# Optimization experiments

Hardware: AMD Instinct MI355X
Metric: run time of the kernel (lower is better)

## Reference

```python
import jax, jax.numpy as jnp
import numpy as np

NA, NW, H = 20000, 100000, 128
DA, DW = 64, 128
E_CR, E_IN, E_CO = 400000, 600000, 300000


def _seg_softmax(logits, seg, n):
    m = jax.ops.segment_max(logits, seg, num_segments=n)
    e = jnp.exp(logits - m[seg])
    s = jax.ops.segment_sum(e, seg, num_segments=n)
    return e / (s[seg] + 1e-16)


def _gat(x_src, x_dst, edge, W, b, a_s, a_d):
    # PyG GATConv, heads=1, concat=False, shared lin for src/dst, add_self_loops=True
    n_src, n_dst = x_src.shape[0], x_dst.shape[0]
    loops = jnp.arange(min(n_src, n_dst), dtype=edge.dtype)
    src = jnp.concatenate([edge[0], loops])
    dst = jnp.concatenate([edge[1], loops])
    hs = x_src @ W            # [n_src, H]
    hd = x_dst @ W            # [n_dst, H]
    logit = jax.nn.leaky_relu((hs @ a_s)[src] + (hd @ a_d)[dst], 0.2)
    alpha = _seg_softmax(logit, dst, n_dst)          # softmax over in-neighborhoods
    out = jax.ops.segment_sum(alpha[:, None] * hs[src], dst, num_segments=n_dst)
    return out + b


def _mlp2(x, w1, b1, w2, b2):
    return jax.nn.relu(x @ w1 + b1) @ w2 + b2


def setup_inputs() -> dict:
    key = jax.random.key(0)
    ks = iter(jax.random.split(key, 40))

    def p(shape, scale=0.1):
        return jax.random.normal(next(ks), shape, jnp.float32) * scale

    def edges(n_src, n_dst, E):
        s = jax.random.randint(next(ks), (E,), 0, n_src, dtype=jnp.int32)
        d = jax.random.randint(next(ks), (E,), 0, n_dst, dtype=jnp.int32)
        d = jnp.where(s == d, (d + 1) % n_dst, d)  # keep input loop-free (PyG strips them)
        return jnp.stack([s, d])

    e_creates = edges(NA, NW, E_CR)
    inp = {
        'artist_feat': jax.random.normal(next(ks), (NA, DA), jnp.float32),
        'work_feat': jax.random.normal(next(ks), (NW, DW), jnp.float32),
        'a_w1': p((DA, H)), 'a_b1': jnp.zeros(H, jnp.float32),
        'a_w2': p((H, H)), 'a_b2': jnp.zeros(H, jnp.float32),
        'w_w1': p((DW, H)), 'w_b1': jnp.zeros(H, jnp.float32),
        'w_w2': p((H, H)), 'w_b2': jnp.zeros(H, jnp.float32),
        'cr_W': p((H, H)), 'cr_b': jnp.zeros(H, jnp.float32), 'cr_as': p((H,)), 'cr_ad': p((H,)),
        'in_W': p((H, H)), 'in_b': jnp.zeros(H, jnp.float32), 'in_as': p((H,)), 'in_ad': p((H,)),
        'co_W': p((H, H)), 'co_b': jnp.zeros(H, jnp.float32), 'co_as': p((H,)), 'co_ad': p((H,)),
        'p_w1': p((2 * H, 256)), 'p_b1': jnp.zeros(256, jnp.float32),
        'p_w2': p((256, 128)), 'p_b2': jnp.zeros(128, jnp.float32),
        'p_w3': p((128, 1)), 'p_b3': jnp.zeros(1, jnp.float32),
        'e_creates': e_creates,
        'e_created_by': jnp.flip(e_creates, axis=0),  # reverse relation [work, artist]
        'e_infl': edges(NW, NW, E_IN),
        'e_collab': edges(NA, NA, E_CO),
    }
    return inp


def reference(artist_feat, work_feat,
              a_w1, a_b1, a_w2, a_b2,
              w_w1, w_b1, w_w2, w_b2,
              cr_W, cr_b, cr_as, cr_ad,
              in_W, in_b, in_as, in_ad,
              co_W, co_b, co_as, co_ad,
              p_w1, p_b1, p_w2, p_b2, p_w3, p_b3,
              e_creates, e_created_by, e_infl, e_collab):
    ax = _mlp2(artist_feat, a_w1, a_b1, a_w2, a_b2)      # [NA, H]
    wx = _mlp2(work_feat, w_w1, w_b1, w_w2, w_b2)        # [NW, H]
    wx = jax.nn.elu(_gat(ax, wx, e_creates, cr_W, cr_b, cr_as, cr_ad))
    wx = jax.nn.elu(_gat(wx, wx, e_infl, in_W, in_b, in_as, in_ad))
    au = _gat(wx, ax, e_created_by, cr_W, cr_b, cr_as, cr_ad)  # no elu (matches source)
    ac = jax.nn.elu(_gat(au, au, e_collab, co_W, co_b, co_as, co_ad))
    comb = jnp.concatenate([au, ac], axis=1)             # [NA, 2H]
    h = jax.nn.relu(comb @ p_w1 + p_b1)                  # dropout is identity in eval
    h = jax.nn.relu(h @ p_w2 + p_b2)
    return (h @ p_w3 + p_b3).squeeze()
```

## Files before the change

kernel.cpp:

```cpp
#include <hip/hip_runtime.h>
#include <hip/hip_bf16.h>
#include <cstddef>

#define NA 20000
#define NW 100000
#define HH 128
#define DA 64
#define E_CR 400000
#define E_IN 600000
#define E_CO 300000

#define ROW1 0
#define ROW2 (NW)
#define ROW3 (2 * NW)
#define ROW4 (2 * NW + NA)
#define NTOT (2 * NW + 2 * NA)
#define ETOTR (E_CR + E_IN + E_CR + E_CO)
#define CAPW 40
#define CAPA 88
#define NPREP (10 * 128 + 1)

typedef short v8s __attribute__((ext_vector_type(8)));
typedef float v4f __attribute__((ext_vector_type(4)));

constexpr int PSLOT = 2 * 128 * 264;

__device__ inline short f2bf(float x) {
    union { float f; unsigned u; } c; c.f = x;
    unsigned r = c.u + 0x7fff + ((c.u >> 16) & 1);
    return (short)(r >> 16);
}
__device__ inline float bf2f(short s) {
    union { unsigned u; float f; } c; c.u = ((unsigned)(unsigned short)s) << 16;
    return c.f;
}
__device__ inline float bfu2f(unsigned short s) {
    union { unsigned u; float f; } c; c.u = ((unsigned)s) << 16;
    return c.f;
}

__device__ inline void split8(const float* xv, v8s& h, v8s& l) {
#pragma unroll
    for (int p = 0; p < 4; ++p) {
        float2 xf; xf.x = xv[2 * p]; xf.y = xv[2 * p + 1];
        __hip_bfloat162 hb = __float22bfloat162_rn(xf);
        float2 hf = __bfloat1622float2(hb);
        float2 lf; lf.x = xf.x - hf.x; lf.y = xf.y - hf.y;
        __hip_bfloat162 lb = __float22bfloat162_rn(lf);
        union { __hip_bfloat162 b; short2 s; } uh, ul;
        uh.b = hb; ul.b = lb;
        h[2 * p] = uh.s.x; h[2 * p + 1] = uh.s.y;
        l[2 * p] = ul.s.x; l[2 * p + 1] = ul.s.y;
    }
}

struct PrepDesc { const float* src; int ldw; int K; };
struct PrepArgs { PrepDesc d[10]; const float* wvW; const float* wvA; float* vd; };
struct EdgeSets { const int* e[4]; int E[4]; int row[4]; int cum[5]; int* pad[4]; int cap[4]; };

__global__ __launch_bounds__(256) void k_prep_append(PrepArgs a, short* __restrict__ out,
                                                    EdgeSets es, int* __restrict__ deg)
{
    if (blockIdx.x < NPREP) {
        if (blockIdx.x == NPREP - 1) {
            __shared__ float sa[HH];
            int t = threadIdx.x;
            if (t < HH) sa[t] = a.wvA[t];
            __syncthreads();
            if (t < HH) {
                float s = 0.f;
                for (int jj = 0; jj < HH; ++jj) s += a.wvW[(size_t)t * HH + jj] * sa[jj];
                a.vd[t] = s;
            }
            return;
        }
        int m = blockIdx.x >> 7;
        int e = (blockIdx.x & 127) * 256 + threadIdx.x;
        PrepDesc dd = a.d[m];
        int K = dd.K;
        int KP = (K <= 128) ? K + 8 : K;
        if (e >= K * 128) return;
        int n = e & 127, k = e >> 7;
        float x = dd.src[(size_t)k * dd.ldw + n];
        short h = f2bf(x);
        short l = f2bf(x - bf2f(h));
        short* base = out + (size_t)m * PSLOT;
        base[n * KP + k] = h;
        base[128 * KP + n * KP + k] = l;
        return;
    }
    int b0 = (blockIdx.x - NPREP) * 1024 + threadIdx.x;
    int s[4], d[4], g[4]; bool ok[4];
#pragma unroll
    for (int u = 0; u < 4; ++u) {
        int i = b0 + u * 256;
        ok[u] = i < es.cum[4];
        s[u] = 0; d[u] = 0; g[u] = 0;
        if (ok[u]) {
            int gi = (i >= es.cum[1]) + (i >= es.cum[2]) + (i >= es.cum[3]);
            int t = i - es.cum[gi];
            s[u] = es.e[gi][t];
            d[u] = es.e[gi][es.E[gi] + t];
            g[u] = gi;
        }
    }
    int p[4];
#pragma unroll
    for (int u = 0; u < 4; ++u) if (ok[u]) p[u] = atomicAdd(&deg[es.row[g[u]] + d[u]], 1);
#pragma unroll
    for (int u = 0; u < 4; ++u)
        if (ok[u] && p[u] < es.cap[g[u]])
            es.pad[g[u]][(size_t)d[u] * es.cap[g[u]] + p[u]] = s[u];
}

template<int K, int ACT, int NSS, int ST, int LDSB, int OBF, int DUAL>
__global__ __launch_bounds__(256, 2) void k_mfma(
    const float* __restrict__ X, int ldx,
    const short* __restrict__ Wp,
    const float* __restrict__ bias,
    float* __restrict__ Y, int ldy, int M,
    const float* __restrict__ v1, float* __restrict__ ss1,
    const float* __restrict__ v2, float* __restrict__ ss2,
    const float* __restrict__ sb)
{
    constexpr int KF = K / 32;
    constexpr int KP = LDSB ? K + 8 : K;
    __shared__ short Bs[LDSB ? 2 * 128 * (K + 8) : 8];
    const int tid = threadIdx.x;
    const int wave = tid >> 6, lane = tid & 63;
    const int l15 = lane & 15, quad = lane >> 4;
    int bid = blockIdx.x;
    if (DUAL) {
        int g0 = gridDim.x >> 1;
        if (bid >= g0) { bid -= g0; Wp += PSLOT; bias += 128; Y += 128; }
    }
    const int wrow = bid * 128 + wave * 32;

    if (LDSB) {
        const float4* src = (const float4*)Wp;
        float4* dst = (float4*)Bs;
        constexpr int total = 2 * 128 * KP / 8;
        for (int i = tid; i < total; i += 256) dst[i] = src[i];
    }

    v4f acc[2][8];
#pragma unroll
    for (int rf = 0; rf < 2; ++rf)
#pragma unroll
        for (int cf = 0; cf < 8; ++cf) acc[rf][cf] = (v4f){0.f, 0.f, 0.f, 0.f};

    if (LDSB) {
        v8s ah[2][KF], al[2][KF];
#pragma unroll
        for (int rf = 0; rf < 2; ++rf) {
            int r = wrow + rf * 16 + l15; if (r >= M) r = M - 1;
            const float* xp = X + (size_t)r * ldx + quad * 8;
#pragma unroll
            for (int kf = 0; kf < KF; ++kf) {
                float xv[8];
                *(float4*)&xv[0] = *(const float4*)(xp + kf * 32);
                *(float4*)&xv[4] = *(const float4*)(xp + kf * 32 + 4);
                split8(xv, ah[rf][kf], al[rf][kf]);
            }
        }
        __syncthreads();
#pragma unroll
        for (int kf = 0; kf < KF; ++kf) {
#pragma unroll
            for (int cf = 0; cf < 8; ++cf) {
                const short* bp = &Bs[(cf * 16 + l15) * KP + kf * 32 + quad * 8];
                v8s bh = *(const v8s*)bp;
                v8s bl = *(const v8s*)(bp + 128 * KP);
#pragma unroll
                for (int rf = 0; rf < 2; ++rf) {
                    acc[rf][cf] = __builtin_amdgcn_mfma_f32_16x16x32_bf16(al[rf][kf], bh, acc[rf][cf], 0, 0, 0);
                    acc[rf][cf] = __builtin_amdgcn_mfma_f32_16x16x32_bf16(ah[rf][kf], bl, acc[rf][cf], 0, 0, 0);
                    acc[rf][cf] = __builtin_amdgcn_mfma_f32_16x16x32_bf16(ah[rf][kf], bh, acc[rf][cf], 0, 0, 0);
                }
            }
        }
    } else {
        for (int kf = 0; kf < KF; ++kf) {
            v8s ah[2], al[2];
#pragma unroll
            for (int rf = 0; rf < 2; ++rf) {
                int r = wrow + rf * 16 + l15; if (r >= M) r = M - 1;
                const float* xp = X + (size_t)r * ldx + kf * 32 + quad * 8;
                float xv[8];
                *(float4*)&xv[0] = *(const float4*)xp;
                *(float4*)&xv[4] = *(const float4*)(xp + 4);
                split8(xv, ah[rf], al[rf]);
            }
#pragma unroll
            for (int cf = 0; cf < 8; ++cf) {
                const short* bp = Wp + (size_t)(cf * 16 + l15) * K + kf * 32 + quad * 8;
                v8s bh = *(const v8s*)bp;
                v8s bl = *(const v8s*)(bp + 128 * KP);
#pragma unroll
                for (int rf = 0; rf < 2; ++rf) {
                    acc[rf][cf] = __builtin_amdgcn_mfma_f32_16x16x32_bf16(al[rf], bh, acc[rf][cf], 0, 0, 0);
                    acc[rf][cf] = __builtin_amdgcn_mfma_f32_16x16x32_bf16(ah[rf], bl, acc[rf][cf], 0, 0, 0);
                    acc[rf][cf] = __builtin_amdgcn_mfma_f32_16x16x32_bf16(ah[rf], bh, acc[rf][cf], 0, 0, 0);
                }
            }
        }
    }

    float bv[8], v1c[8], v2c[8];
#pragma unroll
    for (int cf = 0; cf < 8; ++cf) {
        int col = cf * 16 + l15;
        bv[cf] = bias ? bias[col] : 0.f;
        if (NSS >= 1) v1c[cf] = v1[col];
        if (NSS >= 2) v2c[cf] = v2[col];
    }
    float sbv = (NSS >= 1 && sb) ? sb[0] : 0.f;

#pragma unroll
    for (int rf = 0; rf < 2; ++rf) {
#pragma unroll
        for (int reg = 0; reg < 4; ++reg) {
            int r = wrow + rf * 16 + quad * 4 + reg;
            if (r >= M) continue;
            float p1 = 0.f, p2 = 0.f;
#pragma unroll
            for (int cf = 0; cf < 8; ++cf) {
                float o = acc[rf][cf][reg] + bv[cf];
                if (ACT == 1) o = o > 0.f ? o : 0.f;
                if (NSS >= 1) p1 = fmaf(o, v1c[cf], p1);
                if (NSS >= 2) p2 = fmaf(o, v2c[cf], p2);
                if (ST) {
                    if (OBF) ((unsigned short*)Y)[(size_t)r * ldy + cf * 16 + l15] = (unsigned short)f2bf(o);
                    else     Y[(size_t)r * ldy + cf * 16 + l15] = o;
                }
            }
            if (NSS >= 1) {
#pragma unroll
                for (int w = 1; w < 16; w <<= 1) {
                    p1 += __shfl_xor(p1, w, 64);
                    if (NSS >= 2) p2 += __shfl_xor(p2, w, 64);
                }
                if (l15 == 0) {
                    ss1[r] = p1 + sbv;
                    if (NSS >= 2) ss2[r] = p2;
                }
            }
        }
    }
}

struct MfmaCfg {
    const float* X; int ldx;
    const short* Wp;
    const float* bias;
    float* Y; int ldy; int M;
    int act, nss, obf;
    const float* v1; float* ss1;
    const float* v2; float* ss2;
    int nblocks;
};

__global__ __launch_bounds__(256, 2) void k_mfma2(MfmaCfg c0, MfmaCfg c1)
{
    constexpr int K = 128, KF = 4, KP = 136;
    __shared__ short Bs[2 * 128 * KP];
    const bool first = blockIdx.x < c0.nblocks;
    const MfmaCfg& c = first ? c0 : c1;
    const int bid = first ? blockIdx.x : blockIdx.x - c0.nblocks;
    const int tid = threadIdx.x;
    const int wave = tid >> 6, lane = tid & 63;
    const int l15 = lane & 15, quad = lane >> 4;
    const int wrow = bid * 128 + wave * 32;

    {
        const float4* src = (const float4*)c.Wp;
        float4* dst = (float4*)Bs;
        constexpr int total = 2 * 128 * KP / 8;
        for (int i = tid; i < total; i += 256) dst[i] = src[i];
    }

    v4f acc[2][8];
#pragma unroll
    for (int rf = 0; rf < 2; ++rf)
#pragma unroll
        for (int cf = 0; cf < 8; ++cf) acc[rf][cf] = (v4f){0.f, 0.f, 0.f, 0.f};

    v8s ah[2][KF], al[2][KF];
#pragma unroll
    for (int rf = 0; rf < 2; ++rf) {
        int r = wrow + rf * 16 + l15; if (r >= c.M) r = c.M - 1;
        const float* xp = c.X + (size_t)r * c.ldx + quad * 8;
#pragma unroll
        for (int kf = 0; kf < KF; ++kf) {
            float xv[8];
            *(float4*)&xv[0] = *(const float4*)(xp + kf * 32);
            *(float4*)&xv[4] = *(const float4*)(xp + kf * 32 + 4);
            split8(xv, ah[rf][kf], al[rf][kf]);
        }
    }
    __syncthreads();
#pragma unroll
    for (int kf = 0; kf < KF; ++kf) {
#pragma unroll
        for (int cf = 0; cf < 8; ++cf) {
            const short* bp = &Bs[(cf * 16 + l15) * KP + kf * 32 + quad * 8];
            v8s bh = *(const v8s*)bp;
            v8s bl = *(const v8s*)(bp + 128 * KP);
#pragma unroll
            for (int rf = 0; rf < 2; ++rf) {
                acc[rf][cf] = __builtin_amdgcn_mfma_f32_16x16x32_bf16(al[rf][kf], bh, acc[rf][cf], 0, 0, 0);
                acc[rf][cf] = __builtin_amdgcn_mfma_f32_16x16x32_bf16(ah[rf][kf], bl, acc[rf][cf], 0, 0, 0);
                acc[rf][cf] = __builtin_amdgcn_mfma_f32_16x16x32_bf16(ah[rf][kf], bh, acc[rf][cf], 0, 0, 0);
            }
        }
    }

    float bv[8], v1c[8], v2c[8];
#pragma unroll
    for (int cf = 0; cf < 8; ++cf) {
        int col = cf * 16 + l15;
        bv[cf] = c.bias ? c.bias[col] : 0.f;
        v1c[cf] = (c.nss >= 1) ? c.v1[col] : 0.f;
        v2c[cf] = (c.nss >= 2) ? c.v2[col] : 0.f;
    }

#pragma unroll
    for (int rf = 0; rf < 2; ++rf) {
#pragma unroll
        for (int reg = 0; reg < 4; ++reg) {
            int r = wrow + rf * 16 + quad * 4 + reg;
            if (r >= c.M) continue;
            float p1 = 0.f, p2 = 0.f;
#pragma unroll
            for (int cf = 0; cf < 8; ++cf) {
                float o = acc[rf][cf][reg] + bv[cf];
                if (c.act) o = o > 0.f ? o : 0.f;
                p1 = fmaf(o, v1c[cf], p1);
                p2 = fmaf(o, v2c[cf], p2);
                if (c.obf) ((unsigned short*)c.Y)[(size_t)r * c.ldy + cf * 16 + l15] = (unsigned short)f2bf(o);
                else       c.Y[(size_t)r * c.ldy + cf * 16 + l15] = o;
            }
            if (c.nss >= 1) {
#pragma unroll
                for (int w = 1; w < 16; w <<= 1) {
                    p1 += __shfl_xor(p1, w, 64);
                    p2 += __shfl_xor(p2, w, 64);
                }
                if (l15 == 0) {
                    c.ss1[r] = p1;
                    if (c.nss >= 2) c.ss2[r] = p2;
                }
            }
        }
    }
}

template<int ELU, int U, int CAP>
__global__ __launch_bounds__(256) void k_aggregate(
    const int* __restrict__ deg, const int* __restrict__ esp,
    const unsigned short* __restrict__ hs, const float* __restrict__ ss,
    const float* __restrict__ sd, const float* __restrict__ bias,
    float* __restrict__ out, int ldy, int n, int loopn)
{
    int lane = threadIdx.x & 63;
    int wv = threadIdx.x >> 6;
    int d = blockIdx.x * 4 + wv;
    if (d >= n) return;
    int half = lane >> 5;
    int col = (lane & 31) * 4;
    const int* row = esp + (size_t)d * CAP;
    int i1 = deg[d]; if (i1 > CAP) i1 = CAP;
    float sdv = sd[d];
    float den = 0.f;
    float ax = 0.f, ay = 0.f, az = 0.f, aw = 0.f;
    if (half == 0 && d < loopn) {
        ushort4 h = *(const ushort4*)(hs + (size_t)d * HH + col);
        float l = ss[d] + sdv;
        l = l < 0.f ? 0.2f * l : l;
        float e = __expf(l);
        den += e;
        ax = fmaf(e, bfu2f(h.x), ax);
        ay = fmaf(e, bfu2f(h.y), ay);
        az = fmaf(e, bfu2f(h.z), az);
        aw = fmaf(e, bfu2f(h.w), aw);
    }
    int i = 0;
    for (; i + 2 * U <= i1; i += 2 * U) {
        int s[U]; ushort4 h[U]; float sv[U];
#pragma unroll
        for (int u = 0; u < U; ++u) s[u] = row[i + 2 * u + half];
#pragma unroll
        for (int u = 0; u < U; ++u) h[u] = *(const ushort4*)(hs + (size_t)s[u] * HH + col);
#pragma unroll
        for (int u = 0; u < U; ++u) sv[u] = ss[s[u]];
#pragma unroll
        for (int u = 0; u < U; ++u) {
            float l = sv[u] + sdv;
            l = l < 0.f ? 0.2f * l : l;
            float e = __expf(l);
            den += e;
            ax = fmaf(e, bfu2f(h[u].x), ax);
            ay = fmaf(e, bfu2f(h[u].y), ay);
            az = fmaf(e, bfu2f(h[u].z), az);
            aw = fmaf(e, bfu2f(h[u].w), aw);
        }
    }
    if (i < i1) {
        int s[U]; ushort4 h[U]; float sv[U]; bool act[U];
#pragma unroll
        for (int u = 0; u < U; ++u) {
            int idx = i + 2 * u + half;
            act[u] = idx < i1;
            s[u] = row[act[u] ? idx : (i1 - 1)];
        }
#pragma unroll
        for (int u = 0; u < U; ++u) h[u] = *(const ushort4*)(hs + (size_t)s[u] * HH + col);
#pragma unroll
        for (int u = 0; u < U; ++u) sv[u] = ss[s[u]];
#pragma unroll
        for (int u = 0; u < U; ++u) {
            float l = sv[u] + sdv;
            l = l < 0.f ? 0.2f * l : l;
            float e = act[u] ? __expf(l) : 0.f;
            den += e;
            ax = fmaf(e, bfu2f(h[u].x), ax);
            ay = fmaf(e, bfu2f(h[u].y), ay);
            az = fmaf(e, bfu2f(h[u].z), az);
            aw = fmaf(e, bfu2f(h[u].w), aw);
        }
    }
    den += __shfl_xor(den, 32, 64);
    ax += __shfl_xor(ax, 32, 64);
    ay += __shfl_xor(ay, 32, 64);
    az += __shfl_xor(az, 32, 64);
    aw += __shfl_xor(aw, 32, 64);
    if (half == 0) {
        float4 b = *(const float4*)(bias + col);
        float inv = 1.f / (den + 1e-16f);
        float o0 = ax * inv + b.x;
        float o1 = ay * inv + b.y;
        float o2 = az * inv + b.z;
        float o3 = aw * inv + b.w;
        if (ELU) {
            o0 = o0 > 0.f ? o0 : expm1f(o0);
            o1 = o1 > 0.f ? o1 : expm1f(o1);
            o2 = o2 > 0.f ? o2 : expm1f(o2);
            o3 = o3 > 0.f ? o3 : expm1f(o3);
        }
        *(float4*)(out + (size_t)d * ldy + col) = make_float4(o0, o1, o2, o3);
    }
}

extern "C" void kernel_launch(void* const* d_in, const int* in_sizes, int n_in,
                              void* d_out, int out_size, void* d_ws, size_t ws_size,
                              hipStream_t stream)
{
    const float* artist = (const float*)d_in[0];
    const float* workf  = (const float*)d_in[1];
    const float* a_w1 = (const float*)d_in[2];  const float* a_b1 = (const float*)d_in[3];
    const float* a_w2 = (const float*)d_in[4];  const float* a_b2 = (const float*)d_in[5];
    const float* w_w1 = (const float*)d_in[6];  const float* w_b1 = (const float*)d_in[7];
    const float* w_w2 = (const float*)d_in[8];  const float* w_b2 = (const float*)d_in[9];
    const float* cr_W = (const float*)d_in[10]; const float* cr_b = (const float*)d_in[11];
    const float* cr_as = (const float*)d_in[12]; const float* cr_ad = (const float*)d_in[13];
    const float* in_W = (const float*)d_in[14]; const float* in_b = (const float*)d_in[15];
    const float* in_as = (const float*)d_in[16]; const float* in_ad = (const float*)d_in[17];
    const float* co_W = (const float*)d_in[18]; const float* co_b = (const float*)d_in[19];
    const float* co_as = (const float*)d_in[20]; const float* co_ad = (const float*)d_in[21];
    const float* p_w1 = (const float*)d_in[22]; const float* p_b1 = (const float*)d_in[23];
    const float* p_w2 = (const float*)d_in[24]; const float* p_b2 = (const float*)d_in[25];
    const float* p_w3 = (const float*)d_in[26]; const float* p_b3 = (const float*)d_in[27];
    const int* e_cr = (const int*)d_in[28];
    const int* e_cb = (const int*)d_in[29];
    const int* e_in = (const int*)d_in[30];
    const int* e_co = (const int*)d_in[31];

    char* wsp = (char*)d_ws;
    size_t off = 0;
    auto alloc = [&](size_t bytes) -> void* {
        void* p = wsp + off;
        off += (bytes + 255) / 256 * 256;
        return p;
    };
    float* ax   = (float*)alloc((size_t)NA * HH * 4);
    float* hsA  = (float*)alloc((size_t)NA * HH * 4);
    float* wx   = (float*)alloc((size_t)NW * HH * 4);
    float* hs   = (float*)alloc((size_t)NW * HH * 4);
    unsigned short* hsb = (unsigned short*)alloc((size_t)NW * HH * 2);
    float* comb = (float*)alloc((size_t)NA * 256 * 4);
    float* ss1 = (float*)alloc((size_t)NA * 4);
    float* sd1 = (float*)alloc((size_t)NW * 4);
    float* ss2 = (float*)alloc((size_t)NW * 4);
    float* sd2 = (float*)alloc((size_t)NW * 4);
    float* ss3 = (float*)alloc((size_t)NW * 4);
    float* sd3 = (float*)alloc((size_t)NA * 4);
    float* ss4 = (float*)alloc((size_t)NA * 4);
    float* sd4 = (float*)alloc((size_t)NA * 4);
    float* vd  = (float*)alloc(HH * 4);
    int* deg   = (int*)alloc((size_t)NTOT * 4);
    int* pad1  = (int*)alloc((size_t)NW * CAPW * 4);
    int* pad2  = (int*)alloc((size_t)NW * CAPW * 4);
    int* pad3  = (int*)alloc((size_t)NA * CAPA * 4);
    int* pad4  = (int*)alloc((size_t)NA * CAPA * 4);
    short* preW = (short*)alloc((size_t)10 * PSLOT * 2);
    (void)ws_size; (void)in_sizes; (void)n_in; (void)out_size;

    auto pre = [&](int m) { return preW + (size_t)m * PSLOT; };
    auto gg = [](int M) { return (M + 127) / 128; };
    const float* nf = nullptr;
    float* nfm = nullptr;

    PrepArgs pa;
    pa.d[0] = {a_w1, HH, DA};
    pa.d[1] = {a_w2, HH, HH};
    pa.d[2] = {w_w1, HH, HH};
    pa.d[3] = {w_w2, HH, HH};
    pa.d[4] = {cr_W, HH, HH};
    pa.d[5] = {in_W, HH, HH};
    pa.d[6] = {co_W, HH, HH};
    pa.d[7] = {p_w1, 256, 256};
    pa.d[8] = {p_w1 + 128, 256, 256};
    pa.d[9] = {p_w2, HH, 256};
    pa.wvW = cr_W; pa.wvA = cr_ad; pa.vd = vd;

    EdgeSets es;
    es.e[0] = e_cr; es.e[1] = e_in; es.e[2] = e_cb; es.e[3] = e_co;
    es.E[0] = E_CR; es.E[1] = E_IN; es.E[2] = E_CR; es.E[3] = E_CO;
    es.row[0] = ROW1; es.row[1] = ROW2; es.row[2] = ROW3; es.row[3] = ROW4;
    es.cum[0] = 0; es.cum[1] = E_CR; es.cum[2] = E_CR + E_IN;
    es.cum[3] = E_CR + E_IN + E_CR; es.cum[4] = ETOTR;
    es.pad[0] = pad1; es.pad[1] = pad2; es.pad[2] = pad3; es.pad[3] = pad4;
    es.cap[0] = CAPW; es.cap[1] = CAPW; es.cap[2] = CAPA; es.cap[3] = CAPA;

    (void)hipMemsetAsync(deg, 0, (size_t)NTOT * 4, stream);
    int nApp = (ETOTR + 1023) / 1024;
    k_prep_append<<<NPREP + nApp, 256, 0, stream>>>(pa, preW, es, deg);

    k_mfma<DA, 1, 0, 1, 1, 0, 0><<<gg(NA), 256, 0, stream>>>(artist, DA, pre(0), a_b1, hsA, HH, NA, nf, nfm, nf, nfm, nf);

    {
        MfmaCfg c0 = {workf, HH, pre(2), w_b1, hs, HH, NW, 1, 0, 0, nf, nfm, nf, nfm, gg(NW)};
        MfmaCfg c1 = {hsA, HH, pre(1), a_b2, ax, HH, NA, 0, 1, 0, vd, sd3, nf, nfm, gg(NA)};
        k_mfma2<<<gg(NW) + gg(NA), 256, 0, stream>>>(c0, c1);
    }
    {
        MfmaCfg c0 = {hs, HH, pre(3), w_b2, wx, HH, NW, 0, 1, 0, vd, sd1, nf, nfm, gg(NW)};
        MfmaCfg c1 = {ax, HH, pre(4), nullptr, (float*)hsb, HH, NA, 0, 1, 1, cr_as, ss1, nf, nfm, gg(NA)};
        k_mfma2<<<gg(NW) + gg(NA), 256, 0, stream>>>(c0, c1);
    }

    k_aggregate<1, 2, CAPW><<<(NW + 3) / 4, 256, 0, stream>>>(deg + ROW1, pad1, hsb, ss1, sd1, cr_b, wx, HH, NW, NA);

    k_mfma<HH, 0, 2, 1, 1, 1, 0><<<gg(NW), 256, 0, stream>>>(wx, HH, pre(5), nullptr, (float*)hsb, HH, NW, in_as, ss2, in_ad, sd2, nf);
    k_aggregate<1, 2, CAPW><<<(NW + 3) / 4, 256, 0, stream>>>(deg + ROW2, pad2, hsb, ss2, sd2, in_b, wx, HH, NW, NW);

    k_mfma<HH, 0, 1, 1, 1, 1, 0><<<gg(NW), 256, 0, stream>>>(wx, HH, pre(4), nullptr, (float*)hsb, HH, NW, cr_as, ss3, nf, nfm, nf);
    k_aggregate<0, 4, CAPA><<<(NA + 3) / 4, 256, 0, stream>>>(deg + ROW3, pad3, hsb, ss3, sd3, cr_b, comb, 256, NA, NA);

    k_mfma<HH, 0, 2, 1, 1, 1, 0><<<gg(NA), 256, 0, stream>>>(comb, 256, pre(6), nullptr, (float*)hsb, HH, NA, co_as, ss4, co_ad, sd4, nf);
    k_aggregate<1, 4, CAPA><<<(NA + 3) / 4, 256, 0, stream>>>(deg + ROW4, pad4, hsb, ss4, sd4, co_b, comb + 128, 256, NA, NA);

    float* h1 = hs;
    k_mfma<256, 1, 0, 1, 0, 0, 1><<<2 * gg(NA), 256, 0, stream>>>(comb, 256, pre(7), p_b1, h1, 256, NA, nf, nfm, nf, nfm, nf);
    k_mfma<256, 1, 1, 0, 0, 0, 0><<<gg(NA), 256, 0, stream>>>(h1, 256, pre(9), p_b2, nfm, 0, NA, p_w3, (float*)d_out, nf, nfm, p_b3);
}
```

Baseline: 617.7 us.

## Split edge-append across earlier kernels so each relation is built just in time

The single edge-bucketing pass over all four relations is split into per-relation chunks, and each chunk rides as extra blocks on a kernel that runs before that relation's aggregation (prep, the two dual-MFMA kernels, and the influence-GEMM now launched through the dual kernel). The goal is to shorten the serial prep step and let atomic scatter work overlap with MFMA GEMM blocks. It adds a branch and an extra kernel argument to the MFMA kernel, and mixing the two kinds of block may change occupancy.

```diff
diff --git a/kernel.cpp b/kernel.cpp
--- a/kernel.cpp
+++ b/kernel.cpp
@@ -15,7 +15,6 @@
 #define ROW3 (2 * NW)
 #define ROW4 (2 * NW + NA)
 #define NTOT (2 * NW + 2 * NA)
-#define ETOTR (E_CR + E_IN + E_CR + E_CO)
 #define CAPW 40
 #define CAPA 88
 #define NPREP (10 * 128 + 1)
@@ -54,63 +53,59 @@
     }
 }
 
+struct AppChunk { const int* e; int E; int* pad; int cap; int* deg; };
+
+__device__ inline void do_append(const AppChunk& ap, int bid) {
+    int b0 = bid * 1024 + threadIdx.x;
+    int s[4], d[4]; bool ok[4];
+#pragma unroll
+    for (int u = 0; u < 4; ++u) {
+        int i = b0 + u * 256;
+        ok[u] = i < ap.E;
+        s[u] = 0; d[u] = 0;
+        if (ok[u]) { s[u] = ap.e[i]; d[u] = ap.e[ap.E + i]; }
+    }
+    int p[4];
+#pragma unroll
+    for (int u = 0; u < 4; ++u) if (ok[u]) p[u] = atomicAdd(&ap.deg[d[u]], 1);
+#pragma unroll
+    for (int u = 0; u < 4; ++u)
+        if (ok[u] && p[u] < ap.cap)
+            ap.pad[(size_t)d[u] * ap.cap + p[u]] = s[u];
+}
+
 struct PrepDesc { const float* src; int ldw; int K; };
 struct PrepArgs { PrepDesc d[10]; const float* wvW; const float* wvA; float* vd; };
-struct EdgeSets { const int* e[4]; int E[4]; int row[4]; int cum[5]; int* pad[4]; int cap[4]; };
 
 __global__ __launch_bounds__(256) void k_prep_append(PrepArgs a, short* __restrict__ out,
-                                                    EdgeSets es, int* __restrict__ deg)
+                                                    AppChunk ap)
 {
-    if (blockIdx.x < NPREP) {
-        if (blockIdx.x == NPREP - 1) {
-            __shared__ float sa[HH];
-            int t = threadIdx.x;
-            if (t < HH) sa[t] = a.wvA[t];
-            __syncthreads();
-            if (t < HH) {
-                float s = 0.f;
-                for (int jj = 0; jj < HH; ++jj) s += a.wvW[(size_t)t * HH + jj] * sa[jj];
-                a.vd[t] = s;
-            }
-            return;
-        }
-        int m = blockIdx.x >> 7;
-        int e = (blockIdx.x & 127) * 256 + threadIdx.x;
-        PrepDesc dd = a.d[m];
-        int K = dd.K;
-        int KP = (K <= 128) ? K + 8 : K;
-        if (e >= K * 128) return;
-        int n = e & 127, k = e >> 7;
-        float x = dd.src[(size_t)k * dd.ldw + n];
-        short h = f2bf(x);
-        short l = f2bf(x - bf2f(h));
-        short* base = out + (size_t)m * PSLOT;
-        base[n * KP + k] = h;
-        base[128 * KP + n * KP + k] = l;
+    if (blockIdx.x >= NPREP) { do_append(ap, blockIdx.x - NPREP); return; }
+    if (blockIdx.x == NPREP - 1) {
+        __shared__ float sa[HH];
+        int t = threadIdx.x;
+        if (t < HH) sa[t] = a.wvA[t];
+        __syncthreads();
+        if (t < HH) {
+            float s = 0.f;
+            for (int jj = 0; jj < HH; ++jj) s += a.wvW[(size_t)t * HH + jj] * sa[jj];
+            a.vd[t] = s;
+        }
         return;
     }
-    int b0 = (blockIdx.x - NPREP) * 1024 + threadIdx.x;
-    int s[4], d[4], g[4]; bool ok[4];
-#pragma unroll
-    for (int u = 0; u < 4; ++u) {
-        int i = b0 + u * 256;
-        ok[u] = i < es.cum[4];
-        s[u] = 0; d[u] = 0; g[u] = 0;
-        if (ok[u]) {
-            int gi = (i >= es.cum[1]) + (i >= es.cum[2]) + (i >= es.cum[3]);
-            int t = i - es.cum[gi];
-            s[u] = es.e[gi][t];
-            d[u] = es.e[gi][es.E[gi] + t];
-            g[u] = gi;
-        }
-    }
-    int p[4];
-#pragma unroll
-    for (int u = 0; u < 4; ++u) if (ok[u]) p[u] = atomicAdd(&deg[es.row[g[u]] + d[u]], 1);
-#pragma unroll
-    for (int u = 0; u < 4; ++u)
-        if (ok[u] && p[u] < es.cap[g[u]])
-            es.pad[g[u]][(size_t)d[u] * es.cap[g[u]] + p[u]] = s[u];
+    int m = blockIdx.x >> 7;
+    int e = (blockIdx.x & 127) * 256 + threadIdx.x;
+    PrepDesc dd = a.d[m];
+    int K = dd.K;
+    int KP = (K <= 128) ? K + 8 : K;
+    if (e >= K * 128) return;
+    int n = e & 127, k = e >> 7;
+    float x = dd.src[(size_t)k * dd.ldw + n];
+    short h = f2bf(x);
+    short l = f2bf(x - bf2f(h));
+    short* base = out + (size_t)m * PSLOT;
+    base[n * KP + k] = h;
+    base[128 * KP + n * KP + k] = l;
 }
 
 template<int K, int ACT, int NSS, int ST, int LDSB, int OBF, int DUAL>
@@ -260,13 +255,15 @@
     int nblocks;
 };
 
-__global__ __launch_bounds__(256, 2) void k_mfma2(MfmaCfg c0, MfmaCfg c1)
+__global__ __launch_bounds__(256, 2) void k_mfma2(MfmaCfg c0, MfmaCfg c1, AppChunk ap)
 {
     constexpr int K = 128, KF = 4, KP = 136;
     __shared__ short Bs[2 * 128 * KP];
-    const bool first = blockIdx.x < c0.nblocks;
+    int bid = blockIdx.x;
+    if (bid >= c0.nblocks + c1.nblocks) { do_append(ap, bid - c0.nblocks - c1.nblocks); return; }
+    const bool first = bid < c0.nblocks;
     const MfmaCfg& c = first ? c0 : c1;
-    const int bid = first ? blockIdx.x : blockIdx.x - c0.nblocks;
+    if (!first) bid -= c0.nblocks;
     const int tid = threadIdx.x;
     const int wave = tid >> 6, lane = tid & 63;
     const int l15 = lane & 15, quad = lane >> 4;
@@ -507,6 +504,7 @@
 
     auto pre = [&](int m) { return preW + (size_t)m * PSLOT; };
     auto gg = [](int M) { return (M + 127) / 128; };
+    auto apb = [](int E) { return (E + 1023) / 1024; };
     const float* nf = nullptr;
     float* nfm = nullptr;
 
@@ -523,35 +521,36 @@
     pa.d[9] = {p_w2, HH, 256};
     pa.wvW = cr_W; pa.wvA = cr_ad; pa.vd = vd;
 
-    EdgeSets es;
-    es.e[0] = e_cr; es.e[1] = e_in; es.e[2] = e_cb; es.e[3] = e_co;
-    es.E[0] = E_CR; es.E[1] = E_IN; es.E[2] = E_CR; es.E[3] = E_CO;
-    es.row[0] = ROW1; es.row[1] = ROW2; es.row[2] = ROW3; es.row[3] = ROW4;
-    es.cum[0] = 0; es.cum[1] = E_CR; es.cum[2] = E_CR + E_IN;
-    es.cum[3] = E_CR + E_IN + E_CR; es.cum[4] = ETOTR;
-    es.pad[0] = pad1; es.pad[1] = pad2; es.pad[2] = pad3; es.pad[3] = pad4;
-    es.cap[0] = CAPW; es.cap[1] = CAPW; es.cap[2] = CAPA; es.cap[3] = CAPA;
+    AppChunk ap1 = {e_cr, E_CR, pad1, CAPW, deg + ROW1};
+    AppChunk ap2 = {e_in, E_IN, pad2, CAPW, deg + ROW2};
+    AppChunk ap3 = {e_cb, E_CR, pad3, CAPA, deg + ROW3};
+    AppChunk ap4 = {e_co, E_CO, pad4, CAPA, deg + ROW4};
+    AppChunk ap0 = {nullptr, 0, nullptr, 1, nullptr};
 
     (void)hipMemsetAsync(deg, 0, (size_t)NTOT * 4, stream);
-    int nApp = (ETOTR + 1023) / 1024;
-    k_prep_append<<<NPREP + nApp, 256, 0, stream>>>(pa, preW, es, deg);
+
+    k_prep_append<<<NPREP + apb(E_CR), 256, 0, stream>>>(pa, preW, ap1);
 
     k_mfma<DA, 1, 0, 1, 1, 0, 0><<<gg(NA), 256, 0, stream>>>(artist, DA, pre(0), a_b1, hsA, HH, NA, nf, nfm, nf, nfm, nf);
 
     {
         MfmaCfg c0 = {workf, HH, pre(2), w_b1, hs, HH, NW, 1, 0, 0, nf, nfm, nf, nfm, gg(NW)};
         MfmaCfg c1 = {hsA, HH, pre(1), a_b2, ax, HH, NA, 0, 1, 0, vd, sd3, nf, nfm, gg(NA)};
-        k_mfma2<<<gg(NW) + gg(NA), 256, 0, stream>>>(c0, c1);
+        k_mfma2<<<gg(NW) + gg(NA) + apb(E_IN), 256, 0, stream>>>(c0, c1, ap2);
     }
     {
         MfmaCfg c0 = {hs, HH, pre(3), w_b2, wx, HH, NW, 0, 1, 0, vd, sd1, nf, nfm, gg(NW)};
         MfmaCfg c1 = {ax, HH, pre(4), nullptr, (float*)hsb, HH, NA, 0, 1, 1, cr_as, ss1, nf, nfm, gg(NA)};
-        k_mfma2<<<gg(NW) + gg(NA), 256, 0, stream>>>(c0, c1);
+        k_mfma2<<<gg(NW) + gg(NA) + apb(E_CR), 256, 0, stream>>>(c0, c1, ap3);
     }
 
     k_aggregate<1, 2, CAPW><<<(NW + 3) / 4, 256, 0, stream>>>(deg + ROW1, pad1, hsb, ss1, sd1, cr_b, wx, HH, NW, NA);
 
-    k_mfma<HH, 0, 2, 1, 1, 1, 0><<<gg(NW), 256, 0, stream>>>(wx, HH, pre(5), nullptr, (float*)hsb, HH, NW, in_as, ss2, in_ad, sd2, nf);
+    {
+        MfmaCfg c0 = {wx, HH, pre(5), nullptr, (float*)hsb, HH, NW, 0, 2, 1, in_as, ss2, in_ad, sd2, gg(NW)};
+        MfmaCfg c1 = {nullptr, 0, nullptr, nullptr, nullptr, 0, 0, 0, 0, 0, nf, nfm, nf, nfm, 0};
+        k_mfma2<<<gg(NW) + apb(E_CO), 256, 0, stream>>>(c0, c1, ap4);
+    }
     k_aggregate<1, 2, CAPW><<<(NW + 3) / 4, 256, 0, stream>>>(deg + ROW2, pad2, hsb, ss2, sd2, in_b, wx, HH, NW, NW);
 
     k_mfma<HH, 0, 1, 1, 1, 1, 0><<<gg(NW), 256, 0, stream>>>(wx, HH, pre(4), nullptr, (float*)hsb, HH, NW, cr_as, ss3, nf, nfm, nf);
```

Result: faster. 588.0 us (-4.8%).
